# Optimization experiments

Measured on AMD Instinct MI355X. Metric: run time of the kernel, lower is better.

Reference implementation:

```python
import jax, jax.numpy as jnp
import numpy as np

P = 50          # num_predicates
E = 2000        # num_entities
M = 64          # max_facts_per_query
F = 2_000_000   # num facts
N = 500_000     # num queries
BASE = E + 2    # pack base = max(constant_no, padding_idx) + 2


def setup_inputs() -> dict:
    key = jax.random.key(0)
    k1, k2, k3, k4, k5, k6 = jax.random.split(key, 6)
    fp = jax.random.randint(k1, (F,), 0, P, dtype=jnp.int32)
    fs = jax.random.randint(k2, (F,), 0, E, dtype=jnp.int32)
    fo = jax.random.randint(k3, (F,), 0, E, dtype=jnp.int32)
    facts_idx = jnp.stack([fp, fs, fo], axis=1)  # [F, 3]
    preds = jax.random.randint(k4, (N,), 0, P, dtype=jnp.int32)
    bound_args = jax.random.randint(k5, (N,), 0, E, dtype=jnp.int32)
    direction = jax.random.randint(k6, (N,), 0, 2, dtype=jnp.int32)
    return {"facts_idx": facts_idx, "preds": preds,
            "bound_args": bound_args, "direction": direction}


def _build_csr(keys, vals, num_buckets):
    """Sort vals by key; build offset table via scatter-add + cumsum (as in torch)."""
    order = jnp.argsort(keys)               # stable sort, matches pre-hash-sorted facts
    sorted_vals = vals[order]
    counts = jnp.zeros(num_buckets + 1, dtype=jnp.int32).at[keys + 1].add(1)
    offsets = jnp.cumsum(counts)
    return sorted_vals, offsets


def reference(facts_idx, preds, bound_args, direction):
    # --- _FactIndexBase: sort facts by packed 64-bit hash (lexicographic p,s,o) ---
    fp, fs, fo = facts_idx[:, 0], facts_idx[:, 1], facts_idx[:, 2]
    hashes = (fp * BASE + fs) * BASE + fo   # fits int32 for these dims
    h_order = jnp.argsort(hashes)
    fp, fs, fo = fp[h_order], fs[h_order], fo[h_order]

    # --- _build_inverted_indices: (pred,subj)->objs and (pred,obj)->subjs CSR ---
    ps_sorted_objs, ps_offsets = _build_csr(fp * E + fs, fo, P * E)
    po_sorted_subjs, po_offsets = _build_csr(fp * E + fo, fs, P * E)

    # --- enumerate() ---
    keys = preds * E + bound_args                               # [N]
    starts_ps = ps_offsets[keys]
    counts_ps = jnp.clip(ps_offsets[keys + 1] - starts_ps, 0, M)
    starts_po = po_offsets[keys]
    counts_po = jnp.clip(po_offsets[keys + 1] - starts_po, 0, M)
    is_obj = direction == 0                                     # [N] bool
    starts = jnp.where(is_obj, starts_ps, starts_po)
    counts = jnp.where(is_obj, counts_ps, counts_po)

    pos = jnp.arange(M, dtype=jnp.int32)[None, :]               # [1, M]
    valid = pos < counts[:, None]                               # [N, M]
    size = ps_sorted_objs.shape[0]                              # == F for both arrays
    gi = jnp.clip(starts[:, None] + pos, 0, size - 1)           # [N, M]
    vals_obj = ps_sorted_objs[gi]
    vals_subj = po_sorted_subjs[gi]
    candidates = jnp.where(is_obj[:, None], vals_obj, vals_subj)
    return candidates, valid
```

## Files before the change

kernel.cpp:

```cpp
#include <hip/hip_runtime.h>

#define PCONST 50
#define ECONST 2000
#define MCONST 64
#define NKEY   (PCONST * ECONST)
#define KPB    256
#define NBIN   ((NKEY + KPB - 1) / KPB)
#define NBIN2  (2 * NBIN)
#define SC_THREADS 256
#define SC_CHUNK   8192
#define FPT    (SC_CHUNK / SC_THREADS)
#define CAP    6144

typedef int ivec4 __attribute__((ext_vector_type(4)));

__global__ void __launch_bounds__(SC_THREADS, 1)
scatter_sort(const int* __restrict__ facts,
             int* __restrict__ bincur,
             unsigned* __restrict__ slab, int F) {
    __shared__ unsigned ordered[2 * SC_CHUNK];
    __shared__ int cnt[NBIN2];
    __shared__ int lbase[NBIN2];
    __shared__ int cur[NBIN2];
    __shared__ int base[NBIN2];
    __shared__ int partial[SC_THREADS];

    int t = threadIdx.x;
    int blockStart = blockIdx.x * SC_CHUNK;
    int n = min(SC_CHUNK, F - blockStart);
    if (n <= 0) return;

    for (int i = t; i < NBIN2; i += SC_THREADS) cnt[i] = 0;
    __syncthreads();

    int myBase = blockStart + t * FPT;
    int myN = F - myBase;
    myN = (myN < 0) ? 0 : ((myN > FPT) ? FPT : myN);

    if (myN == FPT) {
        const int4* p = (const int4*)(facts + 3 * myBase);
        #pragma unroll
        for (int k = 0; k < FPT / 4; ++k) {
            int4 a = p[3 * k], b = p[3 * k + 1], c = p[3 * k + 2];
            atomicAdd(&cnt[(a.x * ECONST + a.y) >> 8], 1);
            atomicAdd(&cnt[NBIN + ((a.x * ECONST + a.z) >> 8)], 1);
            atomicAdd(&cnt[(a.w * ECONST + b.x) >> 8], 1);
            atomicAdd(&cnt[NBIN + ((a.w * ECONST + b.y) >> 8)], 1);
            atomicAdd(&cnt[(b.z * ECONST + b.w) >> 8], 1);
            atomicAdd(&cnt[NBIN + ((b.z * ECONST + c.x) >> 8)], 1);
            atomicAdd(&cnt[(c.y * ECONST + c.z) >> 8], 1);
            atomicAdd(&cnt[NBIN + ((c.y * ECONST + c.w) >> 8)], 1);
        }
    } else {
        for (int i = 0; i < myN; ++i) {
            int g = myBase + i;
            int fp = facts[3 * g], fs = facts[3 * g + 1], fo = facts[3 * g + 2];
            atomicAdd(&cnt[(fp * ECONST + fs) >> 8], 1);
            atomicAdd(&cnt[NBIN + ((fp * ECONST + fo) >> 8)], 1);
        }
    }
    __syncthreads();

    {
        int b4 = t * 4;
        int c0 = (b4     < NBIN2) ? cnt[b4]     : 0;
        int c1 = (b4 + 1 < NBIN2) ? cnt[b4 + 1] : 0;
        int c2 = (b4 + 2 < NBIN2) ? cnt[b4 + 2] : 0;
        int c3 = (b4 + 3 < NBIN2) ? cnt[b4 + 3] : 0;
        partial[t] = c0 + c1 + c2 + c3;
        __syncthreads();
        for (int d = 1; d < SC_THREADS; d <<= 1) {
            int v = (t >= d) ? partial[t - d] : 0;
            __syncthreads();
            partial[t] += v;
            __syncthreads();
        }
        int e = (t == 0) ? 0 : partial[t - 1];
        if (b4     < NBIN2) { lbase[b4]     = e; cur[b4]     = e; } e += c0;
        if (b4 + 1 < NBIN2) { lbase[b4 + 1] = e; cur[b4 + 1] = e; } e += c1;
        if (b4 + 2 < NBIN2) { lbase[b4 + 2] = e; cur[b4 + 2] = e; } e += c2;
        if (b4 + 3 < NBIN2) { lbase[b4 + 3] = e; cur[b4 + 3] = e; }
    }
    for (int i = t; i < NBIN2; i += SC_THREADS) {
        int c = cnt[i];
        base[i] = c ? atomicAdd(&bincur[i], c) : 0;
    }
    __syncthreads();

    if (myN == FPT) {
        const int4* p = (const int4*)(facts + 3 * myBase);
        #pragma unroll
        for (int k = 0; k < FPT / 4; ++k) {
            int4 a = p[3 * k], b = p[3 * k + 1], c = p[3 * k + 2];
            int kps, kpo, pos;
            kps = a.x * ECONST + a.y; kpo = a.x * ECONST + a.z;
            pos = atomicAdd(&cur[kps >> 8], 1);
            ordered[pos] = ((unsigned)kps << 11) | (unsigned)a.z;
            pos = atomicAdd(&cur[NBIN + (kpo >> 8)], 1);
            ordered[pos] = (1u << 28) | ((unsigned)kpo << 11) | (unsigned)a.y;
            kps = a.w * ECONST + b.x; kpo = a.w * ECONST + b.y;
            pos = atomicAdd(&cur[kps >> 8], 1);
            ordered[pos] = ((unsigned)kps << 11) | (unsigned)b.y;
            pos = atomicAdd(&cur[NBIN + (kpo >> 8)], 1);
            ordered[pos] = (1u << 28) | ((unsigned)kpo << 11) | (unsigned)b.x;
            kps = b.z * ECONST + b.w; kpo = b.z * ECONST + c.x;
            pos = atomicAdd(&cur[kps >> 8], 1);
            ordered[pos] = ((unsigned)kps << 11) | (unsigned)c.x;
            pos = atomicAdd(&cur[NBIN + (kpo >> 8)], 1);
            ordered[pos] = (1u << 28) | ((unsigned)kpo << 11) | (unsigned)b.w;
            kps = c.y * ECONST + c.z; kpo = c.y * ECONST + c.w;
            pos = atomicAdd(&cur[kps >> 8], 1);
            ordered[pos] = ((unsigned)kps << 11) | (unsigned)c.w;
            pos = atomicAdd(&cur[NBIN + (kpo >> 8)], 1);
            ordered[pos] = (1u << 28) | ((unsigned)kpo << 11) | (unsigned)c.z;
        }
    } else {
        for (int i = 0; i < myN; ++i) {
            int g = myBase + i;
            int fp = facts[3 * g], fs = facts[3 * g + 1], fo = facts[3 * g + 2];
            int kps = fp * ECONST + fs;
            int kpo = fp * ECONST + fo;
            int pos = atomicAdd(&cur[kps >> 8], 1);
            ordered[pos] = ((unsigned)kps << 11) | (unsigned)fo;
            pos = atomicAdd(&cur[NBIN + (kpo >> 8)], 1);
            ordered[pos] = (1u << 28) | ((unsigned)kpo << 11) | (unsigned)fs;
        }
    }
    __syncthreads();

    int n2 = 2 * n;
    for (int j = t; j < n2; j += SC_THREADS) {
        unsigned v = ordered[j];
        int cbin = (int)((v >> 19) & 511u) + ((v >> 28) ? NBIN : 0);
        int pos  = base[cbin] + (j - lbase[cbin]);
        if (pos < CAP) slab[(size_t)cbin * CAP + pos] = v & 0x0FFFFFFFu;
    }
}

__global__ void binsort_kernel(const int* __restrict__ bincur,
                               const unsigned* __restrict__ slab,
                               int* __restrict__ off_ps,
                               int* __restrict__ off_po,
                               unsigned short* __restrict__ data_ps,
                               unsigned short* __restrict__ data_po, int F) {
    __shared__ unsigned buf[CAP];
    __shared__ unsigned short outv[CAP];
    __shared__ int hist[KPB];
    __shared__ int partial[KPB];
    __shared__ int red[4];

    int wg = blockIdx.x;
    int* offout;
    unsigned short* data;
    const int* curbase;
    int b;
    if (wg < NBIN) { offout = off_ps; data = data_ps; curbase = bincur;        b = wg; }
    else           { offout = off_po; data = data_po; curbase = bincur + NBIN; b = wg - NBIN; }
    int t = threadIdx.x;

    int s = 0;
    for (int i = t; i < b; i += KPB) s += curbase[i];
    for (int d = 1; d < 64; d <<= 1) s += __shfl_xor(s, d);
    int lane = t & 63, wv = t >> 6;
    if (lane == 0) red[wv] = s;
    __syncthreads();
    int start = red[0] + red[1] + red[2] + red[3];

    int key0 = b * KPB;
    int len  = min(curbase[b], CAP);
    const unsigned* src = slab + (size_t)wg * CAP;

    if (t == 0 && b == 0) offout[NKEY] = F;

    for (int i = t; i < len; i += KPB) buf[i] = src[i];
    hist[t] = 0;
    __syncthreads();
    for (int i = t; i < len; i += KPB)
        atomicAdd(&hist[(int)(buf[i] >> 11) - key0], 1);
    __syncthreads();

    partial[t] = hist[t];
    __syncthreads();
    for (int d = 1; d < KPB; d <<= 1) {
        int v = (t >= d) ? partial[t - d] : 0;
        __syncthreads();
        partial[t] += v;
        __syncthreads();
    }
    int excl = (t == 0) ? 0 : partial[t - 1];
    int gk = key0 + t;
    if (gk < NKEY) offout[gk] = start + excl;
    hist[t] = excl;
    __syncthreads();

    for (int i = t; i < len; i += KPB) {
        unsigned v = buf[i];
        int lk  = (int)(v >> 11) - key0;
        int pos = atomicAdd(&hist[lk], 1);
        outv[pos] = (unsigned short)(v & 2047u);
    }
    __syncthreads();

    {
        int s0 = (t == 0) ? 0 : hist[t - 1];
        int e0 = hist[t];
        for (int i = s0 + 1; i < e0; ++i) {
            unsigned short v = outv[i]; int j = i - 1;
            while (j >= s0 && outv[j] > v) { outv[j + 1] = outv[j]; --j; }
            outv[j + 1] = v;
        }
    }
    __syncthreads();

    for (int i = t; i < len; i += KPB) data[start + i] = outv[i];
}

__global__ void query_kernel(const int* __restrict__ preds,
                             const int* __restrict__ bound,
                             const int* __restrict__ dir,
                             const int* __restrict__ off_ps,
                             const int* __restrict__ off_po,
                             const unsigned short* __restrict__ vals_ps,
                             const unsigned short* __restrict__ vals_po,
                             int* __restrict__ cand,
                             int* __restrict__ valid, int N, int F) {
    int gwave  = (blockIdx.x * blockDim.x + threadIdx.x) >> 6;
    int lane   = threadIdx.x & 63;
    int nwaves = (gridDim.x * blockDim.x) >> 6;
    int grp = lane >> 4;
    int sl  = (lane & 15) * 4;

    for (int qb = gwave * 64; qb < N; qb += nwaves * 64) {
        int q = qb + lane;
        unsigned pk = 0;
        if (q < N) {
            int key = preds[q] * ECONST + bound[q];
            int dd  = dir[q];
            const int* off = (dd == 0) ? off_ps : off_po;
            int s0 = off[key];
            int c0 = min(off[key + 1] - s0, MCONST);
            if (c0 < 0) c0 = 0;
            pk = ((unsigned)s0 << 9) | ((unsigned)(dd != 0) << 8) | (unsigned)c0;
        }
        int nq = min(64, N - qb);
        for (int j4 = 0; j4 < nq; j4 += 4) {
            int j = j4 + grp;
            unsigned pj = (unsigned)__shfl((int)pk, j);
            if (j < nq) {
                int c  = (int)(pj & 255u);
                int s  = (int)(pj >> 9);
                const unsigned short* vals = (pj & 256u) ? vals_po : vals_ps;
                ivec4 cv, vv;
                int g0 = min(s + sl,     F - 1);
                int g1 = min(s + sl + 1, F - 1);
                int g2 = min(s + sl + 2, F - 1);
                int g3 = min(s + sl + 3, F - 1);
                cv.x = (int)vals[g0];
                cv.y = (int)vals[g1];
                cv.z = (int)vals[g2];
                cv.w = (int)vals[g3];
                vv.x = (sl     < c) ? 1 : 0;
                vv.y = (sl + 1 < c) ? 1 : 0;
                vv.z = (sl + 2 < c) ? 1 : 0;
                vv.w = (sl + 3 < c) ? 1 : 0;
                size_t o = (size_t)(qb + j) * MCONST + sl;
                __builtin_nontemporal_store(cv, (ivec4*)&cand[o]);
                __builtin_nontemporal_store(vv, (ivec4*)&valid[o]);
            }
        }
    }
}

extern "C" void kernel_launch(void* const* d_in, const int* in_sizes, int n_in,
                              void* d_out, int out_size, void* d_ws, size_t ws_size,
                              hipStream_t stream) {
    const int* facts = (const int*)d_in[0];
    const int* preds = (const int*)d_in[1];
    const int* bound = (const int*)d_in[2];
    const int* dir   = (const int*)d_in[3];
    int F = in_sizes[0] / 3;
    int N = in_sizes[1];

    int* ws       = (int*)d_ws;
    int* off_ps   = ws;
    int* off_po   = off_ps + NKEY + 4;
    int* bincur   = off_po + NKEY + 4;
    int* pad      = bincur + NBIN2;
    size_t ofs = (size_t)(pad - ws);
    ofs = (ofs + 3) & ~(size_t)3;
    unsigned short* data_ps = (unsigned short*)(ws + ofs);
    unsigned short* data_po = data_ps + F;
    unsigned* slab = (unsigned*)(data_po + F);

    hipMemsetAsync(bincur, 0, (size_t)NBIN2 * sizeof(int), stream);

    int nChunks = (F + SC_CHUNK - 1) / SC_CHUNK;
    scatter_sort<<<nChunks, SC_THREADS, 0, stream>>>(facts, bincur, slab, F);
    binsort_kernel<<<NBIN2, KPB, 0, stream>>>(bincur, slab,
                                              off_ps, off_po, data_ps, data_po, F);

    int* cand  = (int*)d_out;
    int* valid = cand + (size_t)N * MCONST;
    int qBlocks = (N / 64 + 3) / 4 + 1;
    query_kernel<<<qBlocks, 256, 0, stream>>>(
        preds, bound, dir, off_ps, off_po, data_ps, data_po, cand, valid, N, F);
}
```

Baseline: 163.3 us.

## Split each sort bin across two workgroups and shrink scatter chunks

The binsort kernel now launches two workgroups per bin, each reading the slab directly, building the full key histogram, and then placing and insertion-sorting only its half of the 256 keys. This halves per-workgroup LDS and tail work, which should allow higher occupancy and more parallelism. The cost is that each half reads the whole bin twice from global memory. Separately, the scatter kernel uses 512 threads with 4096-fact chunks and drops the one-block-per-CU launch bound, so more blocks with smaller LDS footprints run at once, at the cost of more global atomics on bincur.

```diff
diff --git a/kernel.cpp b/kernel.cpp
--- a/kernel.cpp
+++ b/kernel.cpp
@@ -7,14 +7,16 @@
 #define KPB    256
 #define NBIN   ((NKEY + KPB - 1) / KPB)
 #define NBIN2  (2 * NBIN)
-#define SC_THREADS 256
-#define SC_CHUNK   8192
+#define SC_THREADS 512
+#define SC_CHUNK   4096
 #define FPT    (SC_CHUNK / SC_THREADS)
 #define CAP    6144
+#define HKEYS  128
+#define HCAP   3328
 
 typedef int ivec4 __attribute__((ext_vector_type(4)));
 
-__global__ void __launch_bounds__(SC_THREADS, 1)
+__global__ void __launch_bounds__(SC_THREADS)
 scatter_sort(const int* __restrict__ facts,
              int* __restrict__ bincur,
              unsigned* __restrict__ slab, int F) {
@@ -62,12 +64,10 @@
     __syncthreads();
 
     {
-        int b4 = t * 4;
-        int c0 = (b4     < NBIN2) ? cnt[b4]     : 0;
-        int c1 = (b4 + 1 < NBIN2) ? cnt[b4 + 1] : 0;
-        int c2 = (b4 + 2 < NBIN2) ? cnt[b4 + 2] : 0;
-        int c3 = (b4 + 3 < NBIN2) ? cnt[b4 + 3] : 0;
-        partial[t] = c0 + c1 + c2 + c3;
+        int b2 = t * 2;
+        int c0 = (b2     < NBIN2) ? cnt[b2]     : 0;
+        int c1 = (b2 + 1 < NBIN2) ? cnt[b2 + 1] : 0;
+        partial[t] = c0 + c1;
         __syncthreads();
         for (int d = 1; d < SC_THREADS; d <<= 1) {
             int v = (t >= d) ? partial[t - d] : 0;
@@ -76,10 +76,8 @@
             __syncthreads();
         }
         int e = (t == 0) ? 0 : partial[t - 1];
-        if (b4     < NBIN2) { lbase[b4]     = e; cur[b4]     = e; } e += c0;
-        if (b4 + 1 < NBIN2) { lbase[b4 + 1] = e; cur[b4 + 1] = e; } e += c1;
-        if (b4 + 2 < NBIN2) { lbase[b4 + 2] = e; cur[b4 + 2] = e; } e += c2;
-        if (b4 + 3 < NBIN2) { lbase[b4 + 3] = e; cur[b4 + 3] = e; }
+        if (b2     < NBIN2) { lbase[b2]     = e; cur[b2]     = e; } e += c0;
+        if (b2 + 1 < NBIN2) { lbase[b2 + 1] = e; cur[b2 + 1] = e; }
     }
     for (int i = t; i < NBIN2; i += SC_THREADS) {
         int c = cnt[i];
@@ -143,19 +141,19 @@
                                int* __restrict__ off_po,
                                unsigned short* __restrict__ data_ps,
                                unsigned short* __restrict__ data_po, int F) {
-    __shared__ unsigned buf[CAP];
-    __shared__ unsigned short outv[CAP];
+    __shared__ unsigned short outv[HCAP];
     __shared__ int hist[KPB];
     __shared__ int partial[KPB];
     __shared__ int red[4];
 
-    int wg = blockIdx.x;
-    int* offout;
-    unsigned short* data;
-    const int* curbase;
-    int b;
-    if (wg < NBIN) { offout = off_ps; data = data_ps; curbase = bincur;        b = wg; }
-    else           { offout = off_po; data = data_po; curbase = bincur + NBIN; b = wg - NBIN; }
+    int wg  = blockIdx.x;
+    int csr = (wg >= 2 * NBIN) ? 1 : 0;
+    int rem = wg - csr * 2 * NBIN;
+    int b   = rem >> 1;
+    int h   = rem & 1;
+    const int* curbase = bincur + csr * NBIN;
+    int* offout             = csr ? off_po  : off_ps;
+    unsigned short* data    = csr ? data_po : data_ps;
     int t = threadIdx.x;
 
     int s = 0;
@@ -164,19 +162,17 @@
     int lane = t & 63, wv = t >> 6;
     if (lane == 0) red[wv] = s;
     __syncthreads();
-    int start = red[0] + red[1] + red[2] + red[3];
-
-    int key0 = b * KPB;
-    int len  = min(curbase[b], CAP);
-    const unsigned* src = slab + (size_t)wg * CAP;
-
-    if (t == 0 && b == 0) offout[NKEY] = F;
-
-    for (int i = t; i < len; i += KPB) buf[i] = src[i];
+    int bin_base = red[0] + red[1] + red[2] + red[3];
+
+    if (b == 0 && h == 0 && t == 0) offout[NKEY] = F;
+
+    int len = min(curbase[b], CAP);
+    const unsigned* src = slab + (size_t)(csr * NBIN + b) * CAP;
+
     hist[t] = 0;
     __syncthreads();
     for (int i = t; i < len; i += KPB)
-        atomicAdd(&hist[(int)(buf[i] >> 11) - key0], 1);
+        atomicAdd(&hist[(int)(src[i] >> 11) & 255], 1);
     __syncthreads();
 
     partial[t] = hist[t];
@@ -187,23 +183,35 @@
         partial[t] += v;
         __syncthreads();
     }
-    int excl = (t == 0) ? 0 : partial[t - 1];
-    int gk = key0 + t;
-    if (gk < NKEY) offout[gk] = start + excl;
-    hist[t] = excl;
+    int k0 = h * HKEYS;
+    int base_excl = (k0 == 0) ? 0 : partial[k0 - 1];
+    int end_excl  = partial[k0 + HKEYS - 1];
+    int len_mine  = min(end_excl - base_excl, HCAP);
+    int start_mine = bin_base + base_excl;
+
+    if (t < HKEYS) {
+        int k = k0 + t;
+        int e = (k == 0) ? 0 : partial[k - 1];
+        offout[b * KPB + k] = bin_base + e;
+    }
+    int e_t = (t == 0) ? 0 : partial[t - 1];
+    hist[t] = e_t - base_excl;
     __syncthreads();
 
     for (int i = t; i < len; i += KPB) {
-        unsigned v = buf[i];
-        int lk  = (int)(v >> 11) - key0;
-        int pos = atomicAdd(&hist[lk], 1);
-        outv[pos] = (unsigned short)(v & 2047u);
-    }
-    __syncthreads();
-
-    {
-        int s0 = (t == 0) ? 0 : hist[t - 1];
-        int e0 = hist[t];
+        unsigned v = src[i];
+        int lk = (int)(v >> 11) & 255;
+        if ((lk >> 7) == h) {
+            int pos = atomicAdd(&hist[lk], 1);
+            if (pos < HCAP) outv[pos] = (unsigned short)(v & 2047u);
+        }
+    }
+    __syncthreads();
+
+    if (t < HKEYS) {
+        int lk = k0 + t;
+        int s0 = (lk == k0) ? 0 : hist[lk - 1];
+        int e0 = min(hist[lk], HCAP);
         for (int i = s0 + 1; i < e0; ++i) {
             unsigned short v = outv[i]; int j = i - 1;
             while (j >= s0 && outv[j] > v) { outv[j + 1] = outv[j]; --j; }
@@ -212,7 +220,7 @@
     }
     __syncthreads();
 
-    for (int i = t; i < len; i += KPB) data[start + i] = outv[i];
+    for (int i = t; i < len_mine; i += KPB) data[start_mine + i] = outv[i];
 }
 
 __global__ void query_kernel(const int* __restrict__ preds,
@@ -296,8 +304,8 @@
 
     int nChunks = (F + SC_CHUNK - 1) / SC_CHUNK;
     scatter_sort<<<nChunks, SC_THREADS, 0, stream>>>(facts, bincur, slab, F);
-    binsort_kernel<<<NBIN2, KPB, 0, stream>>>(bincur, slab,
-                                              off_ps, off_po, data_ps, data_po, F);
+    binsort_kernel<<<4 * NBIN, KPB, 0, stream>>>(bincur, slab,
+                                                 off_ps, off_po, data_ps, data_po, F);
 
     int* cand  = (int*)d_out;
     int* valid = cand + (size_t)N * MCONST;
```

Result: slower. 177.7 us (+8.8%).

## Use 1024-thread blocks in scatter_sort with wave-shuffle bin scan

Applied to the files above, without the earlier changes.

Raises the scatter_sort block from 256 to 1024 threads, so each thread handles 8 facts per chunk instead of 32, and drops the single-block-per-SM launch bound. The bin-offset prefix scan moves from a shared-memory log-step scan with many barriers to per-wavefront shuffle scans plus a small cross-wave sum. The aim is more in-flight work to hide global-load and LDS-atomic latency, and fewer block-wide barriers. The cost is more threads contending on the shared bin counters, and a serial loop over wave sums in each thread.

```diff
diff --git a/kernel.cpp b/kernel.cpp
--- a/kernel.cpp
+++ b/kernel.cpp
@@ -7,14 +7,14 @@
 #define KPB    256
 #define NBIN   ((NKEY + KPB - 1) / KPB)
 #define NBIN2  (2 * NBIN)
-#define SC_THREADS 256
+#define SC_THREADS 1024
 #define SC_CHUNK   8192
 #define FPT    (SC_CHUNK / SC_THREADS)
 #define CAP    6144
 
 typedef int ivec4 __attribute__((ext_vector_type(4)));
 
-__global__ void __launch_bounds__(SC_THREADS, 1)
+__global__ void __launch_bounds__(SC_THREADS)
 scatter_sort(const int* __restrict__ facts,
              int* __restrict__ bincur,
              unsigned* __restrict__ slab, int F) {
@@ -23,7 +23,7 @@
     __shared__ int lbase[NBIN2];
     __shared__ int cur[NBIN2];
     __shared__ int base[NBIN2];
-    __shared__ int partial[SC_THREADS];
+    __shared__ int wsum[16];
 
     int t = threadIdx.x;
     int blockStart = blockIdx.x * SC_CHUNK;
@@ -62,25 +62,24 @@
     __syncthreads();
 
     {
-        int b4 = t * 4;
-        int c0 = (b4     < NBIN2) ? cnt[b4]     : 0;
-        int c1 = (b4 + 1 < NBIN2) ? cnt[b4 + 1] : 0;
-        int c2 = (b4 + 2 < NBIN2) ? cnt[b4 + 2] : 0;
-        int c3 = (b4 + 3 < NBIN2) ? cnt[b4 + 3] : 0;
-        partial[t] = c0 + c1 + c2 + c3;
+        int lane = t & 63, w = t >> 6;
+        int c = (t < NBIN2) ? cnt[t] : 0;
+        int inc = c;
+        for (int d = 1; d < 64; d <<= 1) {
+            int v = __shfl_up(inc, d);
+            if (lane >= d) inc += v;
+        }
+        if (lane == 63) wsum[w] = inc;
         __syncthreads();
-        for (int d = 1; d < SC_THREADS; d <<= 1) {
-            int v = (t >= d) ? partial[t - d] : 0;
-            __syncthreads();
-            partial[t] += v;
-            __syncthreads();
-        }
-        int e = (t == 0) ? 0 : partial[t - 1];
-        if (b4     < NBIN2) { lbase[b4]     = e; cur[b4]     = e; } e += c0;
-        if (b4 + 1 < NBIN2) { lbase[b4 + 1] = e; cur[b4 + 1] = e; } e += c1;
-        if (b4 + 2 < NBIN2) { lbase[b4 + 2] = e; cur[b4 + 2] = e; } e += c2;
-        if (b4 + 3 < NBIN2) { lbase[b4 + 3] = e; cur[b4 + 3] = e; }
-    }
+        if (t < NBIN2) {
+            int wbase = 0;
+            for (int i = 0; i < w; ++i) wbase += wsum[i];
+            int excl = wbase + inc - c;
+            lbase[t] = excl;
+            cur[t]   = excl;
+        }
+    }
+    __syncthreads();
     for (int i = t; i < NBIN2; i += SC_THREADS) {
         int c = cnt[i];
         base[i] = c ? atomicAdd(&bincur[i], c) : 0;
```

New measurement: 154.2 us. 1.06x faster.
